# Kernel optimization log

Measured on AMD Instinct MI355X. Metric: run time of the kernel, lower is better.

Reference implementation:

```python
import jax, jax.numpy as jnp
import numpy as np

D = 1024      # mapped_dim
M = 5         # num_ref_modes
H = 112
W = 112


def setup_inputs() -> dict:
    key = jax.random.key(0)
    ks = jax.random.split(key, 9)
    roi_signal = jax.random.randint(ks[0], (1, 1, H, W), 0, M, dtype=jnp.int32)
    roi_features = jax.random.normal(ks[1], (1, D, H, W), dtype=jnp.float32)
    roi_mask = jax.random.uniform(ks[2], (1, 1, H, W), dtype=jnp.float32)
    s = np.float32(1.0 / np.sqrt(D))
    patch_embed = jax.random.normal(ks[3], (M, D), dtype=jnp.float32) * np.float32(np.sqrt(2.0 / (M + D)))
    Wq = jax.random.normal(ks[4], (D, D), dtype=jnp.float32) * s
    Wk = jax.random.normal(ks[5], (D, D), dtype=jnp.float32) * s
    Wv = jax.random.normal(ks[6], (D, D), dtype=jnp.float32) * s
    bq = jnp.zeros((D,), jnp.float32)
    bk = jnp.zeros((D,), jnp.float32)
    bv = jnp.zeros((D,), jnp.float32)
    conv_w = jax.random.normal(ks[7], (1, D), dtype=jnp.float32) * s  # 1x1 conv, out=1
    conv_b = jnp.zeros((1,), jnp.float32)
    return dict(roi_signal=roi_signal, roi_features=roi_features, roi_mask=roi_mask,
                patch_embed=patch_embed, Wq=Wq, bq=bq, Wk=Wk, bk=bk, Wv=Wv, bv=bv,
                conv_w=conv_w, conv_b=conv_b)


def reference(roi_signal, roi_features, roi_mask, patch_embed, Wq, bq, Wk, bk, Wv, bv, conv_w, conv_b):
    _, _, ROI_H, ROI_W = roi_mask.shape
    d = roi_features.shape[1]
    # ref_embed: one_hot(ref_label) @ patch_embed == gather; (1,1,H,W) -> (1,H,W,D) -> (1,D,H,W)
    pe = jnp.transpose(patch_embed[roi_signal[:, 0]], (0, 3, 1, 2))
    xA = roi_features + pe
    # flatten to tokens: (D, N).T -> (N, D)
    A = xA.reshape(d, -1).T
    O = roi_features.reshape(d, -1).T
    Q = A @ Wq.T + bq
    K = O @ Wk.T + bk
    V = O @ Wv.T + bv
    scores = (Q @ K.T) / jnp.sqrt(jnp.float32(d))        # (N, N) -- dominant intermediate
    attn = jax.nn.softmax(scores, axis=-1)
    out = attn @ V                                        # (N, D)
    # 1x1 conv classification head == per-token dot with conv_w
    seg = (out @ conv_w.T + conv_b).reshape(1, 1, ROI_H, ROI_W)
    return jax.nn.sigmoid(seg.astype(jnp.float32))
```

## Files before the change

### kernel.cpp

```cpp
#include <hip/hip_runtime.h>
#include <math.h>


#define DD 1024
#define NN 12544
#define NSPLIT 10
#define NPART  20
#define NTILES 98

typedef __attribute__((ext_vector_type(8))) short short8;
typedef __attribute__((ext_vector_type(4))) float f32x4;
typedef __attribute__((ext_vector_type(4))) unsigned short ushort4_t;
typedef unsigned short ushort_t;
typedef unsigned int uint32;

__device__ __forceinline__ ushort_t f2bf(float f) {
    union { float f; uint32 u; } v; v.f = f;
    uint32 u = v.u + 0x7FFF + ((v.u >> 16) & 1);
    return (ushort_t)(u >> 16);
}

__device__ __forceinline__ void gload_lds16(const void* g, void* l) {
    __builtin_amdgcn_global_load_lds((const __attribute__((address_space(1))) uint32*)g,
                                     (__attribute__((address_space(3))) uint32*)l, 16, 0, 0);
}

__global__ void k_u(const float* __restrict__ Wv, const float* __restrict__ cw,
                    const float* __restrict__ bv, float* __restrict__ u,
                    float* __restrict__ cptr) {
    const int t = threadIdx.x;
    const int k = blockIdx.x * 256 + t;
    const int d0 = blockIdx.y * 64;
    float acc = 0.f;
#pragma unroll 16
    for (int i = 0; i < 64; ++i) acc += Wv[(size_t)(d0 + i) * DD + k] * cw[d0 + i];
    atomicAdd(&u[k], acc);
    if (blockIdx.x == 0 && t < 64) {
        float ca = bv[d0 + t] * cw[d0 + t];
        for (int off = 32; off > 0; off >>= 1) ca += __shfl_down(ca, off);
        if (t == 0) atomicAdd(cptr, ca);
    }
}

__global__ __launch_bounds__(256)
void k_prep(const float* __restrict__ rf, const int* __restrict__ sig,
            const float* __restrict__ pe, const float* __restrict__ u,
            ushort_t* __restrict__ xo, ushort_t* __restrict__ xa,
            float* __restrict__ vsc) {
    __shared__ ushort_t so[64][136];
    __shared__ ushort_t sa[64][136];
    __shared__ float pel[5 * 128];
    __shared__ float ul[128];
    __shared__ int sigl[64];
    __shared__ f32x4 red[16][16];
    const int t = threadIdx.x;
    const int n0 = blockIdx.x * 64;
    if (t < 64) sigl[t] = sig[n0 + t];
    __syncthreads();
    const int dl = t >> 4, tg = t & 15;
    const int sg[4] = {sigl[tg * 4], sigl[tg * 4 + 1], sigl[tg * 4 + 2], sigl[tg * 4 + 3]};
    const int tok = t >> 2, part = t & 3;
    f32x4 vacc = (f32x4)(0.f);

    for (int c = 0; c < 8; ++c) {
        const int d0 = c * 128;
        for (int i = t; i < 640; i += 256) pel[i] = pe[(i >> 7) * DD + d0 + (i & 127)];
        if (t < 128) ul[t] = u[d0 + t];
        __syncthreads();
#pragma unroll
        for (int s = 0; s < 8; ++s) {
            const int dli = s * 16 + dl;
            const f32x4 x = *(const f32x4*)&rf[(size_t)(d0 + dli) * NN + n0 + tg * 4];
            vacc += x * ul[dli];
            ushort_t oo[4], aa[4];
#pragma unroll
            for (int j = 0; j < 4; ++j) {
                oo[j] = f2bf(x[j]);
                aa[j] = f2bf(x[j] + pel[sg[j] * 128 + dli]);
            }
#pragma unroll
            for (int j = 0; j < 4; ++j) {
                so[tg * 4 + j][dli] = oo[j];
                sa[tg * 4 + j][dli] = aa[j];
            }
        }
        __syncthreads();
#pragma unroll
        for (int i = 0; i < 4; ++i) {
            const int off = part * 32 + i * 8;
            *(short8*)&xo[(size_t)(n0 + tok) * DD + d0 + off] = *(const short8*)&so[tok][off];
            *(short8*)&xa[(size_t)(n0 + tok) * DD + d0 + off] = *(const short8*)&sa[tok][off];
        }
        __syncthreads();
    }
    red[dl][tg] = vacc;
    __syncthreads();
    if (t < 64) {
        float s = 0.f;
#pragma unroll
        for (int i = 0; i < 16; ++i) s += ((const float*)&red[i][t >> 2])[t & 3];
        vsc[n0 + t] = s;
    }
}

__global__ void k_wcast(const float* __restrict__ Wq, const float* __restrict__ Wk,
                        ushort_t* __restrict__ wqb, ushort_t* __restrict__ wkb) {
    const int idx = (blockIdx.x * 256 + threadIdx.x) * 8;
    const float* src = blockIdx.y ? Wk : Wq;
    ushort_t* dst = blockIdx.y ? wkb : wqb;
    f32x4 a = *(const f32x4*)&src[idx];
    f32x4 b = *(const f32x4*)&src[idx + 4];
    short8 o;
#pragma unroll
    for (int j = 0; j < 4; ++j) { o[j] = (short)f2bf(a[j]); o[4 + j] = (short)f2bf(b[j]); }
    *(short8*)&dst[idx] = o;
}

__global__ __launch_bounds__(256, 2)
void k_pgemm(const ushort_t* __restrict__ xb, const ushort_t* __restrict__ wb,
             const float* __restrict__ bias, float scale, ushort_t* __restrict__ outb) {
    __shared__ ushort_t as_[128 * 64];
    __shared__ ushort_t bs_[128 * 64];
    const int t = threadIdx.x;
    const int wv = t >> 6, ln = t & 63;
    const int wr = wv >> 1, wc = wv & 1;
    const int l15 = ln & 15, lhi = ln >> 4;
    const int n0 = blockIdx.x * 128;
    const int m0 = blockIdx.y * 128;
    const int srow = wv * 32;
    const int lr = ln >> 3, lc = ln & 7;
    const int swz = lc ^ lr;

    f32x4 acc[4][4];
#pragma unroll
    for (int a = 0; a < 4; ++a)
#pragma unroll
        for (int b = 0; b < 4; ++b) acc[a][b] = (f32x4)(0.f);

    for (int kk = 0; kk < DD; kk += 64) {
        __syncthreads();
#pragma unroll
        for (int i = 0; i < 4; ++i) {
            const int tok = srow + i * 8 + lr;
            gload_lds16(wb + (size_t)(m0 + tok) * DD + kk + (swz << 3), as_ + (srow + i * 8) * 64);
            gload_lds16(xb + (size_t)(n0 + tok) * DD + kk + (swz << 3), bs_ + (srow + i * 8) * 64);
        }
        __syncthreads();
#pragma unroll
        for (int kp = 0; kp < 2; ++kp) {
            short8 af[4], bf_[4];
#pragma unroll
            for (int mi = 0; mi < 4; ++mi) {
                int r = wr * 64 + mi * 16 + l15;
                int cch = (kp * 4 + lhi) ^ (r & 7);
                af[mi] = *(const short8*)(as_ + r * 64 + cch * 8);
            }
#pragma unroll
            for (int ni = 0; ni < 4; ++ni) {
                int r = wc * 64 + ni * 16 + l15;
                int cch = (kp * 4 + lhi) ^ (r & 7);
                bf_[ni] = *(const short8*)(bs_ + r * 64 + cch * 8);
            }
#pragma unroll
            for (int mi = 0; mi < 4; ++mi)
#pragma unroll
                for (int ni = 0; ni < 4; ++ni)
                    acc[mi][ni] = __builtin_amdgcn_mfma_f32_16x16x32_bf16(
                        af[mi], bf_[ni], acc[mi][ni], 0, 0, 0);
        }
    }
    float bb[4][4];
#pragma unroll
    for (int mi = 0; mi < 4; ++mi) {
        f32x4 b4 = *(const f32x4*)&bias[m0 + wr * 64 + mi * 16 + lhi * 4];
#pragma unroll
        for (int r = 0; r < 4; ++r) bb[mi][r] = b4[r];
    }
#pragma unroll
    for (int mi = 0; mi < 4; ++mi)
#pragma unroll
        for (int ni = 0; ni < 4; ++ni) {
            ushort4_t o;
#pragma unroll
            for (int r = 0; r < 4; ++r) o[r] = f2bf((acc[mi][ni][r] + bb[mi][r]) * scale);
            *(ushort4_t*)&outb[(size_t)(n0 + wc * 64 + ni * 16 + l15) * DD +
                               m0 + wr * 64 + mi * 16 + lhi * 4] = o;
        }
}

__global__ __launch_bounds__(256, 2)
void k_attn(const ushort_t* __restrict__ qb, const ushort_t* __restrict__ kb,
            const float* __restrict__ vsc, float* __restrict__ pm,
            float* __restrict__ pl, float* __restrict__ pa) {
    __shared__ ushort_t qs[128 * 64];
    __shared__ ushort_t ks[128 * 64];
    const int t = threadIdx.x;
    const int wv = t >> 6, ln = t & 63;
    const int wr = wv >> 1, wc = wv & 1;
    const int l15 = ln & 15, lhi = ln >> 4;
    const int m0 = blockIdx.x * 128;
    const int split = blockIdx.y;
    const int srow = wv * 32;
    const int lr = ln >> 3, lc = ln & 7;
    const int swz = lc ^ lr;

    float rm[4][4], rl[4][4], ra[4][4];
#pragma unroll
    for (int a = 0; a < 4; ++a)
#pragma unroll
        for (int b = 0; b < 4; ++b) { rm[a][b] = -INFINITY; rl[a][b] = 0.f; ra[a][b] = 0.f; }

    for (int nt = split; nt < NTILES; nt += NSPLIT) {
        const int n0 = nt * 128;
        f32x4 acc[4][4];
#pragma unroll
        for (int a = 0; a < 4; ++a)
#pragma unroll
            for (int b = 0; b < 4; ++b) acc[a][b] = (f32x4)(0.f);

        for (int kk = 0; kk < DD; kk += 64) {
            __syncthreads();
#pragma unroll
            for (int i = 0; i < 4; ++i) {
                const int tok = srow + i * 8 + lr;
                gload_lds16(qb + (size_t)(m0 + tok) * DD + kk + (swz << 3), qs + (srow + i * 8) * 64);
                gload_lds16(kb + (size_t)(n0 + tok) * DD + kk + (swz << 3), ks + (srow + i * 8) * 64);
            }
            __syncthreads();
#pragma unroll
            for (int kp = 0; kp < 2; ++kp) {
                short8 af[4], bf_[4];
#pragma unroll
                for (int mi = 0; mi < 4; ++mi) {
                    int r = wr * 64 + mi * 16 + l15;
                    int cch = (kp * 4 + lhi) ^ (r & 7);
                    af[mi] = *(const short8*)(qs + r * 64 + cch * 8);
                }
#pragma unroll
                for (int ni = 0; ni < 4; ++ni) {
                    int r = wc * 64 + ni * 16 + l15;
                    int cch = (kp * 4 + lhi) ^ (r & 7);
                    bf_[ni] = *(const short8*)(ks + r * 64 + cch * 8);
                }
#pragma unroll
                for (int mi = 0; mi < 4; ++mi)
#pragma unroll
                    for (int ni = 0; ni < 4; ++ni)
                        acc[mi][ni] = __builtin_amdgcn_mfma_f32_16x16x32_bf16(
                            af[mi], bf_[ni], acc[mi][ni], 0, 0, 0);
            }
        }
        float vv[4];
#pragma unroll
        for (int ni = 0; ni < 4; ++ni) vv[ni] = vsc[n0 + wc * 64 + ni * 16 + l15];
#pragma unroll
        for (int mi = 0; mi < 4; ++mi) {
#pragma unroll
            for (int r = 0; r < 4; ++r) {
                float mx = fmaxf(fmaxf(acc[mi][0][r], acc[mi][1][r]),
                                 fmaxf(acc[mi][2][r], acc[mi][3][r]));
                mx = fmaxf(mx, __shfl_xor(mx, 1));
                mx = fmaxf(mx, __shfl_xor(mx, 2));
                mx = fmaxf(mx, __shfl_xor(mx, 4));
                mx = fmaxf(mx, __shfl_xor(mx, 8));
                const float mnew = fmaxf(rm[mi][r], mx);
                float sp = 0.f, sv = 0.f;
#pragma unroll
                for (int ni = 0; ni < 4; ++ni) {
                    float p = __expf(acc[mi][ni][r] - mnew);
                    sp += p; sv += p * vv[ni];
                }
                sp += __shfl_xor(sp, 1); sv += __shfl_xor(sv, 1);
                sp += __shfl_xor(sp, 2); sv += __shfl_xor(sv, 2);
                sp += __shfl_xor(sp, 4); sv += __shfl_xor(sv, 4);
                sp += __shfl_xor(sp, 8); sv += __shfl_xor(sv, 8);
                const float f = __expf(rm[mi][r] - mnew);
                rl[mi][r] = rl[mi][r] * f + sp;
                ra[mi][r] = ra[mi][r] * f + sv;
                rm[mi][r] = mnew;
            }
        }
    }
    if (l15 == 0) {
        const size_t slab = (size_t)(split * 2 + wc) * NN;
#pragma unroll
        for (int mi = 0; mi < 4; ++mi)
#pragma unroll
            for (int r = 0; r < 4; ++r) {
                int row = m0 + wr * 64 + mi * 16 + lhi * 4 + r;
                pm[slab + row] = rm[mi][r];
                pl[slab + row] = rl[mi][r];
                pa[slab + row] = ra[mi][r];
            }
    }
}

__global__ void k_comb(const float* __restrict__ pm, const float* __restrict__ pl,
                       const float* __restrict__ pa, const float* __restrict__ cptr,
                       const float* __restrict__ cb, float* __restrict__ out) {
    int n = blockIdx.x * 256 + threadIdx.x;
    float gm = -INFINITY;
#pragma unroll
    for (int s = 0; s < NPART; ++s) gm = fmaxf(gm, pm[(size_t)s * NN + n]);
    float l = 0.f, a = 0.f;
#pragma unroll
    for (int s = 0; s < NPART; ++s) {
        float f = __expf(pm[(size_t)s * NN + n] - gm);
        l += pl[(size_t)s * NN + n] * f;
        a += pa[(size_t)s * NN + n] * f;
    }
    float x = a / l + cptr[0] + cb[0];
    out[n] = 1.f / (1.f + __expf(-x));
}

extern "C" void kernel_launch(void* const* d_in, const int* in_sizes, int n_in,
                              void* d_out, int out_size, void* d_ws, size_t ws_size,
                              hipStream_t stream) {
    const int* sig = (const int*)d_in[0];
    const float* rf = (const float*)d_in[1];
    const float* pe = (const float*)d_in[3];
    const float* Wq = (const float*)d_in[4];
    const float* bq = (const float*)d_in[5];
    const float* Wk = (const float*)d_in[6];
    const float* bk = (const float*)d_in[7];
    const float* Wv = (const float*)d_in[8];
    const float* bv = (const float*)d_in[9];
    const float* cw = (const float*)d_in[10];
    const float* cb = (const float*)d_in[11];
    float* out = (float*)d_out;

    ushort_t* buf0 = (ushort_t*)d_ws;
    ushort_t* buf1 = buf0 + (size_t)NN * DD;
    ushort_t* buf2 = buf1 + (size_t)NN * DD;
    ushort_t* wqb = buf2 + (size_t)NN * DD;
    ushort_t* wkb = wqb + (size_t)DD * DD;
    float* u = (float*)(wkb + (size_t)DD * DD);
    float* cptr = u + 1024;
    float* vsc = u + 1024 + 16;
    float* pm = vsc + NN;
    float* pl = pm + (size_t)NPART * NN;
    float* pa = pl + (size_t)NPART * NN;

    hipMemsetAsync(u, 0, (1024 + 16) * sizeof(float), stream);
    k_u<<<dim3(4, 16), 256, 0, stream>>>(Wv, cw, bv, u, cptr);
    k_prep<<<196, 256, 0, stream>>>(rf, sig, pe, u, buf0, buf1, vsc);
    k_wcast<<<dim3(512, 2), 256, 0, stream>>>(Wq, Wk, wqb, wkb);
    k_pgemm<<<dim3(98, 8), 256, 0, stream>>>(buf0, wkb, bk, 1.0f, buf2);
    k_pgemm<<<dim3(98, 8), 256, 0, stream>>>(buf1, wqb, bq, 0.03125f, buf0);
    k_attn<<<dim3(98, NSPLIT), 256, 0, stream>>>(buf0, buf2, vsc, pm, pl, pa);
    k_comb<<<NN / 256, 256, 0, stream>>>(pm, pl, pa, cptr, cb, out);
}
```

Measured before the change: 569.3 us.

## Enlarge attention tiles to 256x256 with double-buffered LDS prefetch and XCD remap

The QK^T attention kernel now uses 256x256 tiles with 512 threads (8 waves, each computing 64x128) instead of 128x128 with 256 threads. The K loop runs in 32-wide steps and double-buffers shared memory, prefetching the next slice (including the first slice of the next N tile) while MFMAs run on the current one. Block IDs are remapped across the 8 XCDs, and the split count is halved. The intent is more operand reuse per LDS load and hidden global-load latency, at the cost of more accumulator registers and fewer blocks (245) to keep CUs busy.

```diff
diff --git a/kernel.cpp b/kernel.cpp
--- a/kernel.cpp
+++ b/kernel.cpp
@@ -4,9 +4,9 @@
 
 #define DD 1024
 #define NN 12544
-#define NSPLIT 10
-#define NPART  20
-#define NTILES 98
+#define NSPLIT 5
+#define NPART  10
+#define NTILES 49
 
 typedef __attribute__((ext_vector_type(8))) short short8;
 typedef __attribute__((ext_vector_type(4))) float f32x4;
@@ -188,21 +188,25 @@
         }
 }
 
-__global__ __launch_bounds__(256, 2)
+__global__ __launch_bounds__(512, 2)
 void k_attn(const ushort_t* __restrict__ qb, const ushort_t* __restrict__ kb,
             const float* __restrict__ vsc, float* __restrict__ pm,
             float* __restrict__ pl, float* __restrict__ pa) {
-    __shared__ ushort_t qs[128 * 64];
-    __shared__ ushort_t ks[128 * 64];
+    __shared__ ushort_t As[2][256 * 32];
+    __shared__ ushort_t Bs[2][256 * 32];
     const int t = threadIdx.x;
     const int wv = t >> 6, ln = t & 63;
-    const int wr = wv >> 1, wc = wv & 1;
+    const int wm = wv >> 1, wn = wv & 1;
     const int l15 = ln & 15, lhi = ln >> 4;
-    const int m0 = blockIdx.x * 128;
-    const int split = blockIdx.y;
-    const int srow = wv * 32;
-    const int lr = ln >> 3, lc = ln & 7;
-    const int swz = lc ^ lr;
+
+    const int g = blockIdx.x;
+    const int xcd = g & 7, gq = g >> 3;
+    const int L = (xcd < 5) ? xcd * 31 + gq : 155 + (xcd - 5) * 30 + gq;
+    const int bx = L / NSPLIT, split = L % NSPLIT;
+    const int m0 = bx * 256;
+
+    const int srow0 = (ln >> 2);
+    const int spc = ln & 3;
 
     float rm[4][4], rl[4][4], ra[4][4];
 #pragma unroll
@@ -210,55 +214,81 @@
 #pragma unroll
         for (int b = 0; b < 4; ++b) { rm[a][b] = -INFINITY; rl[a][b] = 0.f; ra[a][b] = 0.f; }
 
+    f32x4 acc[4][8];
+#pragma unroll
+    for (int a = 0; a < 4; ++a)
+#pragma unroll
+        for (int b = 0; b < 8; ++b) acc[a][b] = (f32x4)(0.f);
+
+    int cur = 0;
+    {
+        const int n0 = split * 256;
+#pragma unroll
+        for (int s2 = 0; s2 < 2; ++s2) {
+            const int seg = wv * 2 + s2;
+            const int row = seg * 16 + srow0;
+            const int c = spc ^ ((row >> 1) & 3);
+            gload_lds16(qb + (size_t)(m0 + row) * DD + c * 8, &As[0][seg * 512]);
+            gload_lds16(kb + (size_t)(n0 + row) * DD + c * 8, &Bs[0][seg * 512]);
+        }
+    }
+    __syncthreads();
+
     for (int nt = split; nt < NTILES; nt += NSPLIT) {
-        const int n0 = nt * 128;
-        f32x4 acc[4][4];
-#pragma unroll
-        for (int a = 0; a < 4; ++a)
-#pragma unroll
-            for (int b = 0; b < 4; ++b) acc[a][b] = (f32x4)(0.f);
-
-        for (int kk = 0; kk < DD; kk += 64) {
+        const int n0 = nt * 256;
+        for (int kidx = 0; kidx < 32; ++kidx) {
+            int nk = kidx + 1, nnt = nt;
+            if (nk == 32) { nk = 0; nnt = nt + NSPLIT; }
+            if (nnt < NTILES) {
+                const int nn0 = nnt * 256;
+                const int kko = nk * 32;
+                ushort_t* Ad = &As[cur ^ 1][0];
+                ushort_t* Bd = &Bs[cur ^ 1][0];
+#pragma unroll
+                for (int s2 = 0; s2 < 2; ++s2) {
+                    const int seg = wv * 2 + s2;
+                    const int row = seg * 16 + srow0;
+                    const int c = spc ^ ((row >> 1) & 3);
+                    gload_lds16(qb + (size_t)(m0 + row) * DD + kko + c * 8, Ad + seg * 512);
+                    gload_lds16(kb + (size_t)(nn0 + row) * DD + kko + c * 8, Bd + seg * 512);
+                }
+            }
+            const ushort_t* Ab = &As[cur][0];
+            const ushort_t* Bb = &Bs[cur][0];
+            short8 af[4], bfr[8];
+#pragma unroll
+            for (int mi = 0; mi < 4; ++mi) {
+                const int row = wm * 64 + mi * 16 + l15;
+                const int phys = lhi ^ ((row >> 1) & 3);
+                af[mi] = *(const short8*)(Ab + row * 32 + phys * 8);
+            }
+#pragma unroll
+            for (int ni = 0; ni < 8; ++ni) {
+                const int row = wn * 128 + ni * 16 + l15;
+                const int phys = lhi ^ ((row >> 1) & 3);
+                bfr[ni] = *(const short8*)(Bb + row * 32 + phys * 8);
+            }
+            __builtin_amdgcn_s_setprio(1);
+#pragma unroll
+            for (int ni = 0; ni < 8; ++ni)
+#pragma unroll
+                for (int mi = 0; mi < 4; ++mi)
+                    acc[mi][ni] = __builtin_amdgcn_mfma_f32_16x16x32_bf16(
+                        af[mi], bfr[ni], acc[mi][ni], 0, 0, 0);
+            __builtin_amdgcn_s_setprio(0);
             __syncthreads();
-#pragma unroll
-            for (int i = 0; i < 4; ++i) {
-                const int tok = srow + i * 8 + lr;
-                gload_lds16(qb + (size_t)(m0 + tok) * DD + kk + (swz << 3), qs + (srow + i * 8) * 64);
-                gload_lds16(kb + (size_t)(n0 + tok) * DD + kk + (swz << 3), ks + (srow + i * 8) * 64);
-            }
-            __syncthreads();
-#pragma unroll
-            for (int kp = 0; kp < 2; ++kp) {
-                short8 af[4], bf_[4];
-#pragma unroll
-                for (int mi = 0; mi < 4; ++mi) {
-                    int r = wr * 64 + mi * 16 + l15;
-                    int cch = (kp * 4 + lhi) ^ (r & 7);
-                    af[mi] = *(const short8*)(qs + r * 64 + cch * 8);
-                }
-#pragma unroll
-                for (int ni = 0; ni < 4; ++ni) {
-                    int r = wc * 64 + ni * 16 + l15;
-                    int cch = (kp * 4 + lhi) ^ (r & 7);
-                    bf_[ni] = *(const short8*)(ks + r * 64 + cch * 8);
-                }
-#pragma unroll
-                for (int mi = 0; mi < 4; ++mi)
-#pragma unroll
-                    for (int ni = 0; ni < 4; ++ni)
-                        acc[mi][ni] = __builtin_amdgcn_mfma_f32_16x16x32_bf16(
-                            af[mi], bf_[ni], acc[mi][ni], 0, 0, 0);
-            }
-        }
-        float vv[4];
-#pragma unroll
-        for (int ni = 0; ni < 4; ++ni) vv[ni] = vsc[n0 + wc * 64 + ni * 16 + l15];
+            cur ^= 1;
+        }
+        float vv[8];
+#pragma unroll
+        for (int ni = 0; ni < 8; ++ni) vv[ni] = vsc[n0 + wn * 128 + ni * 16 + l15];
 #pragma unroll
         for (int mi = 0; mi < 4; ++mi) {
 #pragma unroll
             for (int r = 0; r < 4; ++r) {
-                float mx = fmaxf(fmaxf(acc[mi][0][r], acc[mi][1][r]),
-                                 fmaxf(acc[mi][2][r], acc[mi][3][r]));
+                float mx = acc[mi][0][r];
+#pragma unroll
+                for (int ni = 1; ni < 8; ++ni) mx = fmaxf(mx, acc[mi][ni][r]);
                 mx = fmaxf(mx, __shfl_xor(mx, 1));
                 mx = fmaxf(mx, __shfl_xor(mx, 2));
                 mx = fmaxf(mx, __shfl_xor(mx, 4));
@@ -266,7 +296,7 @@
                 const float mnew = fmaxf(rm[mi][r], mx);
                 float sp = 0.f, sv = 0.f;
 #pragma unroll
-                for (int ni = 0; ni < 4; ++ni) {
+                for (int ni = 0; ni < 8; ++ni) {
                     float p = __expf(acc[mi][ni][r] - mnew);
                     sp += p; sv += p * vv[ni];
                 }
@@ -280,14 +310,18 @@
                 rm[mi][r] = mnew;
             }
         }
+#pragma unroll
+        for (int a = 0; a < 4; ++a)
+#pragma unroll
+            for (int b = 0; b < 8; ++b) acc[a][b] = (f32x4)(0.f);
     }
     if (l15 == 0) {
-        const size_t slab = (size_t)(split * 2 + wc) * NN;
+        const size_t slab = (size_t)(split * 2 + wn) * NN;
 #pragma unroll
         for (int mi = 0; mi < 4; ++mi)
 #pragma unroll
             for (int r = 0; r < 4; ++r) {
-                int row = m0 + wr * 64 + mi * 16 + lhi * 4 + r;
+                int row = m0 + wm * 64 + mi * 16 + lhi * 4 + r;
                 pm[slab + row] = rm[mi][r];
                 pl[slab + row] = rl[mi][r];
                 pa[slab + row] = ra[mi][r];
@@ -347,6 +381,6 @@
     k_wcast<<<dim3(512, 2), 256, 0, stream>>>(Wq, Wk, wqb, wkb);
     k_pgemm<<<dim3(98, 8), 256, 0, stream>>>(buf0, wkb, bk, 1.0f, buf2);
     k_pgemm<<<dim3(98, 8), 256, 0, stream>>>(buf1, wqb, bq, 0.03125f, buf0);
-    k_attn<<<dim3(98, NSPLIT), 256, 0, stream>>>(buf0, buf2, vsc, pm, pl, pa);
+    k_attn<<<245, 512, 0, stream>>>(buf0, buf2, vsc, pm, pl, pa);
     k_comb<<<NN / 256, 256, 0, stream>>>(pm, pl, pa, cptr, cb, out);
 }
```

New measurement: 541.5 us. 1.05x faster.
